# Kernel optimization log

Hardware: AMD Instinct MI355X
Metric: run time of the kernel (lower is better)

The kernel has to match this reference:

```python
import jax, jax.numpy as jnp
import numpy as np

B, Q, D = 4, 8192, 256
H, L, P = 8, 4, 4
HD = D // H
SPATIAL = [(128, 128), (64, 64), (32, 32), (16, 16)]


def setup_inputs() -> dict:
    key = jax.random.key(0)
    ks = jax.random.split(key, 12)
    inp = {
        "query": jax.random.normal(ks[0], (B, Q, D), jnp.float32),
        "feat0": jax.random.normal(ks[1], (B, D) + SPATIAL[0], jnp.float32),
        "feat1": jax.random.normal(ks[2], (B, D) + SPATIAL[1], jnp.float32),
        "feat2": jax.random.normal(ks[3], (B, D) + SPATIAL[2], jnp.float32),
        "feat3": jax.random.normal(ks[4], (B, D) + SPATIAL[3], jnp.float32),
        "reference_points": jax.random.uniform(ks[5], (B, Q, 2), jnp.float32),
        "W_off": jax.random.normal(ks[6], (D, H * L * P * 2), jnp.float32) * 0.02,
        "b_off": jnp.zeros((H * L * P * 2,), jnp.float32),
        "W_attn": jax.random.normal(ks[7], (D, H * L * P), jnp.float32) * 0.02,
        "b_attn": jnp.zeros((H * L * P,), jnp.float32),
        "W_out": jax.random.normal(ks[8], (D, D), jnp.float32) * 0.02,
        "b_out": jnp.zeros((D,), jnp.float32),
    }
    return inp


def _bilinear_sample(img, grid):
    # img: (C, Hf, Wf); grid: (N, 2) with (x, y) in [-1, 1]; align_corners=True,
    # padding_mode='zeros' semantics (out-of-range corners contribute 0).
    C, Hf, Wf = img.shape
    x = (grid[:, 0] + 1.0) * 0.5 * (Wf - 1)
    y = (grid[:, 1] + 1.0) * 0.5 * (Hf - 1)
    x0 = jnp.floor(x)
    y0 = jnp.floor(y)
    x1 = x0 + 1.0
    y1 = y0 + 1.0
    wx1 = x - x0
    wx0 = 1.0 - wx1
    wy1 = y - y0
    wy0 = 1.0 - wy1

    def gather(xi, yi):
        valid = (xi >= 0) & (xi <= Wf - 1) & (yi >= 0) & (yi <= Hf - 1)
        xc = jnp.clip(xi, 0, Wf - 1).astype(jnp.int32)
        yc = jnp.clip(yi, 0, Hf - 1).astype(jnp.int32)
        return img[:, yc, xc] * valid.astype(img.dtype)  # (C, N)

    out = (gather(x0, y0) * (wx0 * wy0)
           + gather(x1, y0) * (wx1 * wy0)
           + gather(x0, y1) * (wx0 * wy1)
           + gather(x1, y1) * (wx1 * wy1))
    return out  # (C, N)


_sample_bh = jax.vmap(_bilinear_sample)  # over fused (B*H) axis


def _msdeform(query, feats, reference_points,
              W_off, b_off, W_attn, b_attn, W_out, b_out):
    offsets = jnp.tanh(query @ W_off + b_off).reshape(B, Q, H, L, P, 2)
    logits = (query @ W_attn + b_attn).reshape(B, Q, H, L * P)
    attn = jax.nn.softmax(logits, axis=3).reshape(B, Q, H, L, P)
    ref_grid = reference_points * 2.0 - 1.0  # (B, Q, 2)

    agg = jnp.zeros((B, Q, H, HD), dtype=query.dtype)
    for lvl, feat in enumerate(feats):
        Hf, Wf = feat.shape[2], feat.shape[3]
        img = feat.reshape(B * H, HD, Hf, Wf)
        # (B, H, Q, P, 2)
        grid = ref_grid[:, None, :, None, :] + jnp.transpose(
            offsets[:, :, :, lvl], (0, 2, 1, 3, 4))
        grid = grid.reshape(B * H, Q * P, 2)
        samp = _sample_bh(img, grid).reshape(B, H, HD, Q, P)
        agg = agg + jnp.einsum('bhcqp,bqhp->bqhc', samp, attn[:, :, :, lvl, :])

    out = agg.reshape(B, Q, D) @ W_out + b_out
    return out, attn


def reference(query, feat0, feat1, feat2, feat3, reference_points,
              W_off, b_off, W_attn, b_attn, W_out, b_out):
    return _msdeform(query, [feat0, feat1, feat2, feat3], reference_points,
                     W_off, b_off, W_attn, b_attn, W_out, b_out)
```

## Files before the change

### kernel.cpp

```cpp
#include <hip/hip_runtime.h>
#include <cstdint>
#include <cstddef>

#define NB 4
#define NQ 8192
#define ND 256
#define NH 8
#define NL 4
#define NP 4
#define QBLK 16

__global__ __launch_bounds__(256) void transpose_k(
    const float* __restrict__ in, float* __restrict__ out, int HW) {
  __shared__ float tile[32][33];
  int yx0 = blockIdx.x << 5;
  int d0  = blockIdx.y << 5;
  int b   = blockIdx.z;
  const float* inb = in + (size_t)b * ND * HW;
  float* outb = out + (size_t)b * HW * ND;
  int col = threadIdx.x & 31;
  int row = threadIdx.x >> 5;
#pragma unroll
  for (int r = 0; r < 4; ++r) {
    int d = row + (r << 3);
    tile[d][col] = inb[(size_t)(d0 + d) * HW + (yx0 + col)];
  }
  __syncthreads();
#pragma unroll
  for (int r = 0; r < 4; ++r) {
    int y = row + (r << 3);
    outb[(size_t)(yx0 + y) * ND + (d0 + col)] = tile[col][y];
  }
}

__global__ __launch_bounds__(192) void proj_k(
    const float* __restrict__ query, const float* __restrict__ refp,
    const float* __restrict__ W_off, const float* __restrict__ b_off,
    const float* __restrict__ W_attn, const float* __restrict__ b_attn,
    float* __restrict__ pos, float* __restrict__ attn_out) {
  int q0 = blockIdx.x * QBLK;
  __shared__ float qs[QBLK][ND];
  __shared__ float lg[QBLK][128];
  int t = threadIdx.x;
  {
    const float4* qsrc = (const float4*)(query + (size_t)q0 * ND);
    float4* qdst = (float4*)&qs[0][0];
#pragma unroll
    for (int i = 0; i < 6; ++i) {
      int idx = t + 192 * i;
      if (idx < QBLK * ND / 4) qdst[idx] = qsrc[idx];
    }
  }
  __syncthreads();
  if (t < 128) {
    int slot = t & 63, qg = t >> 6;
    int j0 = slot << 2;
    float4 bb = *(const float4*)(b_off + j0);
    float4 acc[8];
#pragma unroll
    for (int qq = 0; qq < 8; ++qq) acc[qq] = bb;
    const float* qbase = &qs[qg * 8][0];
#pragma unroll 4
    for (int k = 0; k < ND; ++k) {
      float4 w = *(const float4*)(W_off + (size_t)k * 256 + j0);
#pragma unroll
      for (int qq = 0; qq < 8; ++qq) {
        float qk = qbase[qq * ND + k];
        acc[qq].x = fmaf(qk, w.x, acc[qq].x);
        acc[qq].y = fmaf(qk, w.y, acc[qq].y);
        acc[qq].z = fmaf(qk, w.z, acc[qq].z);
        acc[qq].w = fmaf(qk, w.w, acc[qq].w);
      }
    }
#pragma unroll
    for (int qq = 0; qq < 8; ++qq) {
      int bq = q0 + qg * 8 + qq;
      float rx = refp[bq * 2 + 0] * 2.f - 1.f;
      float ry = refp[bq * 2 + 1] * 2.f - 1.f;
      float4 r;
      r.x = rx + tanhf(acc[qq].x);
      r.y = ry + tanhf(acc[qq].y);
      r.z = rx + tanhf(acc[qq].z);
      r.w = ry + tanhf(acc[qq].w);
      *(float4*)(pos + (size_t)bq * 256 + j0) = r;
    }
  } else {
    int u = t - 128;
    int slot = u & 31, qg = u >> 5;
    int j0 = slot << 2;
    float4 bb = *(const float4*)(b_attn + j0);
    float4 acc[8];
#pragma unroll
    for (int qq = 0; qq < 8; ++qq) acc[qq] = bb;
    const float* qbase = &qs[qg * 8][0];
#pragma unroll 4
    for (int k = 0; k < ND; ++k) {
      float4 w = *(const float4*)(W_attn + (size_t)k * 128 + j0);
#pragma unroll
      for (int qq = 0; qq < 8; ++qq) {
        float qk = qbase[qq * ND + k];
        acc[qq].x = fmaf(qk, w.x, acc[qq].x);
        acc[qq].y = fmaf(qk, w.y, acc[qq].y);
        acc[qq].z = fmaf(qk, w.z, acc[qq].z);
        acc[qq].w = fmaf(qk, w.w, acc[qq].w);
      }
    }
#pragma unroll
    for (int qq = 0; qq < 8; ++qq) {
      int qi = qg * 8 + qq;
      lg[qi][j0 + 0] = acc[qq].x;
      lg[qi][j0 + 1] = acc[qq].y;
      lg[qi][j0 + 2] = acc[qq].z;
      lg[qi][j0 + 3] = acc[qq].w;
    }
  }
  __syncthreads();
  if (t < 128) {
    int qi = t >> 3;
    int h = t & 7;
    float* l = &lg[qi][h * 16];
    float m = -1e30f;
#pragma unroll
    for (int i = 0; i < 16; ++i) m = fmaxf(m, l[i]);
    float e[16], s = 0.f;
#pragma unroll
    for (int i = 0; i < 16; ++i) { e[i] = __expf(l[i] - m); s += e[i]; }
    float inv = 1.f / s;
#pragma unroll
    for (int i = 0; i < 16; ++i) l[i] = e[i] * inv;
  }
  __syncthreads();
  {
    const float4* src = (const float4*)&lg[0][0];
    float4* dst = (float4*)(attn_out + (size_t)q0 * 128);
#pragma unroll
    for (int i = 0; i < 3; ++i) {
      int idx = t + 192 * i;
      if (idx < QBLK * 128 / 4) dst[idx] = src[idx];
    }
  }
}

#define HPAD 136
__global__ __launch_bounds__(256) void sample_k(
    const float* __restrict__ feat_ws, const float* __restrict__ pos,
    const float* __restrict__ attnw, float* __restrict__ agg) {
  __shared__ int tbl[4 * NH * HPAD];
  int bid = blockIdx.x;
  int wk = ((bid & 7) << 10) | (bid >> 3);
  int q0 = wk << 2;
  int b = wk >> 11;
  int t = threadIdx.x;

  const int FT1 = NB * 16384 * ND;
  const int FT2 = FT1 + NB * 4096 * ND;
  const int FT3 = FT2 + NB * 1024 * ND;
  int lb[4] = {b * 16384 * ND, FT1 + b * 4096 * ND, FT2 + b * 1024 * ND,
               FT3 + b * 256 * ND};

#pragma unroll
  for (int j = t; j < 512; j += 256) {
    int qi = j >> 7, i = j & 127;
    int bq = q0 + qi;
    float gx = pos[(size_t)bq * 256 + 2 * i];
    float gy = pos[(size_t)bq * 256 + 2 * i + 1];
    float a = attnw[(size_t)bq * 128 + i];
    int l = (i >> 2) & 3;
    int Wf = 128 >> l;
    float wf1 = (float)(Wf - 1);
    float x = (gx + 1.f) * 0.5f * wf1;
    float y = (gy + 1.f) * 0.5f * wf1;
    float x0f = floorf(x), y0f = floorf(y);
    float wx1 = x - x0f, wx0 = 1.f - wx1;
    float wy1 = y - y0f, wy0 = 1.f - wy1;
    int x0 = (int)x0f, y0 = (int)y0f;
    int x1 = x0 + 1, y1 = y0 + 1;
    bool vx0 = (x0 >= 0) && (x0 < Wf);
    bool vx1 = (x1 >= 0) && (x1 < Wf);
    bool vy0 = (y0 >= 0) && (y0 < Wf);
    bool vy1 = (y1 >= 0) && (y1 < Wf);
    int xc0 = min(max(x0, 0), Wf - 1), xc1 = min(max(x1, 0), Wf - 1);
    int yc0 = min(max(y0, 0), Wf - 1), yc1 = min(max(y1, 0), Wf - 1);
    int base = lb[l];
    int o00 = base + (yc0 * Wf + xc0) * ND;
    int o10 = base + (yc0 * Wf + xc1) * ND;
    int o01 = base + (yc1 * Wf + xc0) * ND;
    int o11 = base + (yc1 * Wf + xc1) * ND;
    float w00 = (vx0 && vy0) ? a * wx0 * wy0 : 0.f;
    float w10 = (vx1 && vy0) ? a * wx1 * wy0 : 0.f;
    float w01 = (vx0 && vy1) ? a * wx0 * wy1 : 0.f;
    float w11 = (vx1 && vy1) ? a * wx1 * wy1 : 0.f;
    int h = i >> 4, s = i & 15;
    int* rec = &tbl[(qi * NH + h) * HPAD + s * 8];
    rec[0] = o00; rec[1] = __float_as_int(w00);
    rec[2] = o10; rec[3] = __float_as_int(w10);
    rec[4] = o01; rec[5] = __float_as_int(w01);
    rec[6] = o11; rec[7] = __float_as_int(w11);
  }
  __syncthreads();

  int lane = t & 63, qi = t >> 6;
  int h = lane >> 3, cq = lane & 7;
  int bq = q0 + qi;
  int choff = (h << 5) + (cq << 2);
  const int* rec = &tbl[(qi * NH + h) * HPAD];
  float4 acc = {0.f, 0.f, 0.f, 0.f};
#pragma unroll 4
  for (int s = 0; s < 16; ++s) {
#pragma unroll
    for (int c = 0; c < 4; ++c) {
      int off = rec[s * 8 + c * 2];
      float w = __int_as_float(rec[s * 8 + c * 2 + 1]);
      float4 v = *(const float4*)(feat_ws + off + choff);
      acc.x = fmaf(w, v.x, acc.x);
      acc.y = fmaf(w, v.y, acc.y);
      acc.z = fmaf(w, v.z, acc.z);
      acc.w = fmaf(w, v.w, acc.w);
    }
  }
  *(float4*)(agg + (size_t)bq * 256 + choff) = acc;
}

__global__ __launch_bounds__(128) void out_k(
    const float* __restrict__ agg, const float* __restrict__ W_out,
    const float* __restrict__ b_out, float* __restrict__ out) {
  int q0 = blockIdx.x * QBLK;
  __shared__ float as_[QBLK][ND];
  int t = threadIdx.x;
  {
    const float4* src = (const float4*)(agg + (size_t)q0 * ND);
    float4* dst = (float4*)&as_[0][0];
#pragma unroll
    for (int i = 0; i < 8; ++i) dst[t + 128 * i] = src[t + 128 * i];
  }
  __syncthreads();
  int slot = t & 63, qg = t >> 6;
  int j0 = slot << 2;
  float4 bb = *(const float4*)(b_out + j0);
  float4 acc[8];
#pragma unroll
  for (int qq = 0; qq < 8; ++qq) acc[qq] = bb;
  const float* abase = &as_[qg * 8][0];
#pragma unroll 4
  for (int k = 0; k < ND; ++k) {
    float4 w = *(const float4*)(W_out + (size_t)k * 256 + j0);
#pragma unroll
    for (int qq = 0; qq < 8; ++qq) {
      float ak = abase[qq * ND + k];
      acc[qq].x = fmaf(ak, w.x, acc[qq].x);
      acc[qq].y = fmaf(ak, w.y, acc[qq].y);
      acc[qq].z = fmaf(ak, w.z, acc[qq].z);
      acc[qq].w = fmaf(ak, w.w, acc[qq].w);
    }
  }
#pragma unroll
  for (int qq = 0; qq < 8; ++qq) {
    *(float4*)(out + (size_t)(q0 + qg * 8 + qq) * 256 + j0) = acc[qq];
  }
}

extern "C" void kernel_launch(void* const* d_in, const int* in_sizes, int n_in,
                              void* d_out, int out_size, void* d_ws,
                              size_t ws_size, hipStream_t stream) {
  const float* query  = (const float*)d_in[0];
  const float* feat0  = (const float*)d_in[1];
  const float* feat1  = (const float*)d_in[2];
  const float* feat2  = (const float*)d_in[3];
  const float* feat3  = (const float*)d_in[4];
  const float* refp   = (const float*)d_in[5];
  const float* W_off  = (const float*)d_in[6];
  const float* b_off  = (const float*)d_in[7];
  const float* W_attn = (const float*)d_in[8];
  const float* b_attn = (const float*)d_in[9];
  const float* W_out  = (const float*)d_in[10];
  const float* b_out  = (const float*)d_in[11];

  float* out = (float*)d_out;
  float* attn_out = out + (size_t)NB * NQ * ND;

  float* ws  = (float*)d_ws;
  float* fT0 = ws;
  float* fT1 = fT0 + (size_t)NB * 16384 * ND;
  float* fT2 = fT1 + (size_t)NB * 4096 * ND;
  float* fT3 = fT2 + (size_t)NB * 1024 * ND;
  float* pos = fT3 + (size_t)NB * 256 * ND;
  float* agg = pos + (size_t)NB * NQ * ND;

  transpose_k<<<dim3(512, 8, NB), 256, 0, stream>>>(feat0, fT0, 16384);
  transpose_k<<<dim3(128, 8, NB), 256, 0, stream>>>(feat1, fT1, 4096);
  transpose_k<<<dim3(32, 8, NB), 256, 0, stream>>>(feat2, fT2, 1024);
  transpose_k<<<dim3(8, 8, NB), 256, 0, stream>>>(feat3, fT3, 256);

  proj_k<<<dim3(NB * NQ / QBLK), 192, 0, stream>>>(query, refp, W_off, b_off,
                                                   W_attn, b_attn, pos,
                                                   attn_out);
  sample_k<<<dim3(NB * NQ / 4), 256, 0, stream>>>(fT0, pos, attn_out, agg);
  out_k<<<dim3(NB * NQ / QBLK), 128, 0, stream>>>(agg, W_out, b_out, out);
}
```

Baseline: 467.0 us.

## Drop LDS staging in projection GEMMs and enlarge per-wave query tiles

```diff
diff --git a/kernel.cpp b/kernel.cpp
--- a/kernel.cpp
+++ b/kernel.cpp
@@ -8,7 +8,8 @@
 #define NH 8
 #define NL 4
 #define NP 4
-#define QBLK 16
+#define PQB 32
+#define OQB 64
 
 __global__ __launch_bounds__(256) void transpose_k(
     const float* __restrict__ in, float* __restrict__ out, int HW) {
@@ -33,48 +34,37 @@
   }
 }
 
-__global__ __launch_bounds__(192) void proj_k(
+__global__ __launch_bounds__(256) void proj_k(
     const float* __restrict__ query, const float* __restrict__ refp,
     const float* __restrict__ W_off, const float* __restrict__ b_off,
     const float* __restrict__ W_attn, const float* __restrict__ b_attn,
     float* __restrict__ pos, float* __restrict__ attn_out) {
-  int q0 = blockIdx.x * QBLK;
-  __shared__ float qs[QBLK][ND];
-  __shared__ float lg[QBLK][128];
+  int q0 = blockIdx.x * PQB;
+  __shared__ float lg[PQB][128];
   int t = threadIdx.x;
-  {
-    const float4* qsrc = (const float4*)(query + (size_t)q0 * ND);
-    float4* qdst = (float4*)&qs[0][0];
-#pragma unroll
-    for (int i = 0; i < 6; ++i) {
-      int idx = t + 192 * i;
-      if (idx < QBLK * ND / 4) qdst[idx] = qsrc[idx];
-    }
-  }
-  __syncthreads();
-  if (t < 128) {
-    int slot = t & 63, qg = t >> 6;
-    int j0 = slot << 2;
+  int wave = t >> 6, lane = t & 63;
+  if (wave < 2) {
+    const float* qb = query + (size_t)(q0 + wave * 16) * ND;
+    int j0 = lane << 2;
     float4 bb = *(const float4*)(b_off + j0);
-    float4 acc[8];
-#pragma unroll
-    for (int qq = 0; qq < 8; ++qq) acc[qq] = bb;
-    const float* qbase = &qs[qg * 8][0];
-#pragma unroll 4
+    float4 acc[16];
+#pragma unroll
+    for (int qq = 0; qq < 16; ++qq) acc[qq] = bb;
+#pragma unroll 2
     for (int k = 0; k < ND; ++k) {
       float4 w = *(const float4*)(W_off + (size_t)k * 256 + j0);
 #pragma unroll
-      for (int qq = 0; qq < 8; ++qq) {
-        float qk = qbase[qq * ND + k];
-        acc[qq].x = fmaf(qk, w.x, acc[qq].x);
-        acc[qq].y = fmaf(qk, w.y, acc[qq].y);
-        acc[qq].z = fmaf(qk, w.z, acc[qq].z);
-        acc[qq].w = fmaf(qk, w.w, acc[qq].w);
+      for (int qq = 0; qq < 16; ++qq) {
+        float qv = qb[qq * ND + k];
+        acc[qq].x = fmaf(qv, w.x, acc[qq].x);
+        acc[qq].y = fmaf(qv, w.y, acc[qq].y);
+        acc[qq].z = fmaf(qv, w.z, acc[qq].z);
+        acc[qq].w = fmaf(qv, w.w, acc[qq].w);
       }
     }
 #pragma unroll
-    for (int qq = 0; qq < 8; ++qq) {
-      int bq = q0 + qg * 8 + qq;
+    for (int qq = 0; qq < 16; ++qq) {
+      int bq = q0 + wave * 16 + qq;
       float rx = refp[bq * 2 + 0] * 2.f - 1.f;
       float ry = refp[bq * 2 + 1] * 2.f - 1.f;
       float4 r;
@@ -85,39 +75,31 @@
       *(float4*)(pos + (size_t)bq * 256 + j0) = r;
     }
   } else {
-    int u = t - 128;
-    int slot = u & 31, qg = u >> 5;
-    int j0 = slot << 2;
-    float4 bb = *(const float4*)(b_attn + j0);
-    float4 acc[8];
-#pragma unroll
-    for (int qq = 0; qq < 8; ++qq) acc[qq] = bb;
-    const float* qbase = &qs[qg * 8][0];
-#pragma unroll 4
+    const float* qb = query + (size_t)(q0 + (wave - 2) * 16) * ND;
+    int j0 = lane << 1;
+    float2 bb = *(const float2*)(b_attn + j0);
+    float2 acc[16];
+#pragma unroll
+    for (int qq = 0; qq < 16; ++qq) acc[qq] = bb;
+#pragma unroll 2
     for (int k = 0; k < ND; ++k) {
-      float4 w = *(const float4*)(W_attn + (size_t)k * 128 + j0);
-#pragma unroll
-      for (int qq = 0; qq < 8; ++qq) {
-        float qk = qbase[qq * ND + k];
-        acc[qq].x = fmaf(qk, w.x, acc[qq].x);
-        acc[qq].y = fmaf(qk, w.y, acc[qq].y);
-        acc[qq].z = fmaf(qk, w.z, acc[qq].z);
-        acc[qq].w = fmaf(qk, w.w, acc[qq].w);
+      float2 w = *(const float2*)(W_attn + (size_t)k * 128 + j0);
+#pragma unroll
+      for (int qq = 0; qq < 16; ++qq) {
+        float qv = qb[qq * ND + k];
+        acc[qq].x = fmaf(qv, w.x, acc[qq].x);
+        acc[qq].y = fmaf(qv, w.y, acc[qq].y);
       }
     }
 #pragma unroll
-    for (int qq = 0; qq < 8; ++qq) {
-      int qi = qg * 8 + qq;
-      lg[qi][j0 + 0] = acc[qq].x;
-      lg[qi][j0 + 1] = acc[qq].y;
-      lg[qi][j0 + 2] = acc[qq].z;
-      lg[qi][j0 + 3] = acc[qq].w;
-    }
-  }
-  __syncthreads();
-  if (t < 128) {
-    int qi = t >> 3;
-    int h = t & 7;
+    for (int qq = 0; qq < 16; ++qq) {
+      int qi = (wave - 2) * 16 + qq;
+      *(float2*)&lg[qi][j0] = acc[qq];
+    }
+  }
+  __syncthreads();
+  {
+    int qi = t >> 3, h = t & 7;
     float* l = &lg[qi][h * 16];
     float m = -1e30f;
 #pragma unroll
@@ -134,10 +116,7 @@
     const float4* src = (const float4*)&lg[0][0];
     float4* dst = (float4*)(attn_out + (size_t)q0 * 128);
 #pragma unroll
-    for (int i = 0; i < 3; ++i) {
-      int idx = t + 192 * i;
-      if (idx < QBLK * 128 / 4) dst[idx] = src[idx];
-    }
+    for (int i = 0; i < 4; ++i) dst[t + 256 * i] = src[t + 256 * i];
   }
 }
 
@@ -221,41 +200,33 @@
   *(float4*)(agg + (size_t)bq * 256 + choff) = acc;
 }
 
-__global__ __launch_bounds__(128) void out_k(
+__global__ __launch_bounds__(256) void out_k(
     const float* __restrict__ agg, const float* __restrict__ W_out,
     const float* __restrict__ b_out, float* __restrict__ out) {
-  int q0 = blockIdx.x * QBLK;
-  __shared__ float as_[QBLK][ND];
+  int q0 = blockIdx.x * OQB;
   int t = threadIdx.x;
-  {
-    const float4* src = (const float4*)(agg + (size_t)q0 * ND);
-    float4* dst = (float4*)&as_[0][0];
-#pragma unroll
-    for (int i = 0; i < 8; ++i) dst[t + 128 * i] = src[t + 128 * i];
-  }
-  __syncthreads();
-  int slot = t & 63, qg = t >> 6;
-  int j0 = slot << 2;
+  int wave = t >> 6, lane = t & 63;
+  const float* ab = agg + (size_t)(q0 + wave * 16) * ND;
+  int j0 = lane << 2;
   float4 bb = *(const float4*)(b_out + j0);
-  float4 acc[8];
-#pragma unroll
-  for (int qq = 0; qq < 8; ++qq) acc[qq] = bb;
-  const float* abase = &as_[qg * 8][0];
-#pragma unroll 4
+  float4 acc[16];
+#pragma unroll
+  for (int qq = 0; qq < 16; ++qq) acc[qq] = bb;
+#pragma unroll 2
   for (int k = 0; k < ND; ++k) {
     float4 w = *(const float4*)(W_out + (size_t)k * 256 + j0);
 #pragma unroll
-    for (int qq = 0; qq < 8; ++qq) {
-      float ak = abase[qq * ND + k];
-      acc[qq].x = fmaf(ak, w.x, acc[qq].x);
-      acc[qq].y = fmaf(ak, w.y, acc[qq].y);
-      acc[qq].z = fmaf(ak, w.z, acc[qq].z);
-      acc[qq].w = fmaf(ak, w.w, acc[qq].w);
-    }
-  }
-#pragma unroll
-  for (int qq = 0; qq < 8; ++qq) {
-    *(float4*)(out + (size_t)(q0 + qg * 8 + qq) * 256 + j0) = acc[qq];
+    for (int qq = 0; qq < 16; ++qq) {
+      float av = ab[qq * ND + k];
+      acc[qq].x = fmaf(av, w.x, acc[qq].x);
+      acc[qq].y = fmaf(av, w.y, acc[qq].y);
+      acc[qq].z = fmaf(av, w.z, acc[qq].z);
+      acc[qq].w = fmaf(av, w.w, acc[qq].w);
+    }
+  }
+#pragma unroll
+  for (int qq = 0; qq < 16; ++qq) {
+    *(float4*)(out + (size_t)(q0 + wave * 16 + qq) * 256 + j0) = acc[qq];
   }
 }
 
@@ -291,9 +262,9 @@
   transpose_k<<<dim3(32, 8, NB), 256, 0, stream>>>(feat2, fT2, 1024);
   transpose_k<<<dim3(8, 8, NB), 256, 0, stream>>>(feat3, fT3, 256);
 
-  proj_k<<<dim3(NB * NQ / QBLK), 192, 0, stream>>>(query, refp, W_off, b_off,
-                                                   W_attn, b_attn, pos,
-                                                   attn_out);
+  proj_k<<<dim3(NB * NQ / PQB), 256, 0, stream>>>(query, refp, W_off, b_off,
+                                                  W_attn, b_attn, pos,
+                                                  attn_out);
   sample_k<<<dim3(NB * NQ / 4), 256, 0, stream>>>(fT0, pos, attn_out, agg);
-  out_k<<<dim3(NB * NQ / QBLK), 128, 0, stream>>>(agg, W_out, b_out, out);
-}
+  out_k<<<dim3(NB * NQ / OQB), 256, 0, stream>>>(agg, W_out, b_out, out);
+}
```

Result: slower. 707.2 us (+51.4%).
